# Optimization experiments

Measured on AMD Instinct MI355X. Metric: run time of the kernel, lower is better.

## Reference

```python
import jax, jax.numpy as jnp
import numpy as np

N_NODES = 10000
N_EDGES = 320000
IN_DIM = 256
OUT_DIM = 256
LN_EPS = 1e-5


def setup_inputs() -> dict:
    key = jax.random.key(0)
    ks = jax.random.split(key, 4)
    x = jax.random.normal(ks[0], (N_NODES, IN_DIM), dtype=jnp.float32)
    edge_index = jax.random.randint(ks[1], (2, N_EDGES), 0, N_NODES, dtype=jnp.int64)
    # Linear weights stored input-major so y = x @ W + b
    W_msg = jax.random.normal(ks[2], (2 * IN_DIM, OUT_DIM), dtype=jnp.float32) / np.sqrt(2 * IN_DIM)
    b_msg = jnp.zeros((OUT_DIM,), dtype=jnp.float32)
    W_upd = jax.random.normal(ks[3], (IN_DIM + OUT_DIM, OUT_DIM), dtype=jnp.float32) / np.sqrt(IN_DIM + OUT_DIM)
    b_upd = jnp.zeros((OUT_DIM,), dtype=jnp.float32)
    gamma = jnp.ones((OUT_DIM,), dtype=jnp.float32)
    beta = jnp.zeros((OUT_DIM,), dtype=jnp.float32)
    return {"x": x, "edge_index": edge_index, "W_msg": W_msg, "b_msg": b_msg,
            "W_upd": W_upd, "b_upd": b_upd, "gamma": gamma, "beta": beta}


def reference(x, edge_index, W_msg, b_msg, W_upd, b_upd, gamma, beta):
    row, col = edge_index[0], edge_index[1]
    # gather -> concat -> linear -> relu   [E, out_dim]
    msg_in = jnp.concatenate([x[row], x[col]], axis=-1)
    messages = jax.nn.relu(msg_in @ W_msg + b_msg)
    # scatter-add aggregate over destination nodes  [N, out_dim]
    aggregated = jax.ops.segment_sum(messages, col, num_segments=x.shape[0])
    # update: concat -> linear -> relu -> layernorm
    h = jax.nn.relu(jnp.concatenate([x, aggregated], axis=-1) @ W_upd + b_upd)
    mu = jnp.mean(h, axis=-1, keepdims=True)
    var = jnp.mean(jnp.square(h - mu), axis=-1, keepdims=True)
    return (h - mu) * jax.lax.rsqrt(var + LN_EPS) * gamma + beta
```

## Files before the change

kernel.cpp:

```cpp
#include <hip/hip_runtime.h>
#include <hip/hip_bf16.h>
#include <stdint.h>

#define NNODES 10000
#define NEDGES 320000
#define DIM    256
#define KTOT   512
#define LN_EPS 1e-5f
#define BCAP   96

typedef __attribute__((ext_vector_type(4))) float f32x4;
typedef __attribute__((ext_vector_type(8))) short bf16x8;

__device__ __forceinline__ ushort f2bf(float f) {
    union { float f; uint32_t u; } v; v.f = f;
    uint32_t r = v.u + 0x7fffu + ((v.u >> 16) & 1u);
    return (ushort)(r >> 16);
}
__device__ __forceinline__ float bf2f(ushort u) {
    union { float f; uint32_t u; } v; v.u = ((uint32_t)u) << 16;
    return v.f;
}

__global__ __launch_bounds__(256)
void prep_all(const float* __restrict__ x, const float* __restrict__ Wm,
              const float* __restrict__ Wu, ushort* __restrict__ xb,
              ushort* __restrict__ Wcat, ushort* __restrict__ Wua,
              int4* __restrict__ cntz) {
    int tid = blockIdx.x * 256 + threadIdx.x;
    if (tid < 2560) cntz[tid] = (int4){0, 0, 0, 0};
    if (tid < 640000) {
        float4 v = reinterpret_cast<const float4*>(x)[tid];
        ushort4 o;
        o.x = f2bf(v.x); o.y = f2bf(v.y); o.z = f2bf(v.z); o.w = f2bf(v.w);
        reinterpret_cast<ushort4*>(xb)[tid] = o;
    } else {
        int t = tid - 640000;
        if (t < 131072) {
            int kk  = t >> 14;
            int rem = t & 16383;
            int g   = rem >> 9;
            int kg  = (rem >> 7) & 3;
            int ml  = (rem >> 3) & 15;
            int j   = rem & 7;
            int k = kk * 32 + kg * 8 + j;
            int n = g * 16 + ml;
            float v = (n < 256) ? Wm[k * DIM + n] : Wm[(k + 256) * DIM + (n - 256)];
            Wcat[t] = f2bf(v);
        } else {
            int rem = t - 131072;
            int kk  = rem >> 13;
            int nt  = (rem >> 9) & 15;
            int kg  = (rem >> 7) & 3;
            int ml  = (rem >> 3) & 15;
            int j   = rem & 7;
            int k = kk * 32 + kg * 8 + j;
            int n = nt * 16 + ml;
            Wua[rem] = f2bf(Wu[k * DIM + n]);
        }
    }
}

__global__ __launch_bounds__(256)
void scatter_uv(const int* __restrict__ eidx, int* __restrict__ cnt,
                int* __restrict__ srow, const ushort* __restrict__ xb,
                const ushort* __restrict__ Wcat, const float* __restrict__ bmsg,
                ushort* __restrict__ Ub, float* __restrict__ Vf) {
    if (blockIdx.x < 1250) {
        int e = blockIdx.x * 256 + threadIdx.x;
        int d = eidx[NEDGES + e];
        int p = atomicAdd(&cnt[d], 1);
        if (p < BCAP) srow[d * BCAP + p] = eidx[e];
        return;
    }
    const int wq   = threadIdx.x >> 6;
    const int lane = threadIdx.x & 63;
    const int ml = lane & 15, kg = lane >> 4;
    const int nb = (blockIdx.x - 1250) * 16;
    const uint arow = (uint)(nb + ml) * DIM;

    f32x4 acc[8];
#pragma unroll
    for (int nt = 0; nt < 8; ++nt) acc[nt] = (f32x4){0.f, 0.f, 0.f, 0.f};

#pragma unroll
    for (int kk = 0; kk < 8; ++kk) {
        bf16x8 a = *reinterpret_cast<const bf16x8*>(xb + arow + kk * 32 + kg * 8);
#pragma unroll
        for (int nt = 0; nt < 8; ++nt) {
            bf16x8 b = *reinterpret_cast<const bf16x8*>(Wcat + kk * 16384 + (wq * 8 + nt) * 512 + lane * 8);
            acc[nt] = __builtin_amdgcn_mfma_f32_16x16x32_bf16(a, b, acc[nt], 0, 0, 0);
        }
    }

    if (wq < 2) {
#pragma unroll
        for (int nt = 0; nt < 8; ++nt) {
            const int col = wq * 128 + nt * 16 + ml;
#pragma unroll
            for (int i = 0; i < 4; ++i)
                Ub[(size_t)(nb + kg * 4 + i) * 256 + col] = f2bf(acc[nt][i]);
        }
    } else {
#pragma unroll
        for (int nt = 0; nt < 8; ++nt) {
            const int col = (wq - 2) * 128 + nt * 16 + ml;
            const float bb = bmsg[col];
#pragma unroll
            for (int i = 0; i < 4; ++i)
                Vf[(size_t)(nb + kg * 4 + i) * 256 + col] = acc[nt][i] + bb;
        }
    }
}

__global__ __launch_bounds__(256)
void edge_node(const ushort* __restrict__ Ub, const float* __restrict__ Vf,
               const int* __restrict__ srow, const int* __restrict__ cnt,
               const ushort* __restrict__ xb, const ushort* __restrict__ Wua,
               const float* __restrict__ bupd, const float* __restrict__ gamma,
               const float* __restrict__ beta, float* __restrict__ out) {
    __shared__ float aggS[8][260];
    __shared__ float pS[16][4][2];

    const int tid  = threadIdx.x;
    const int wave = tid >> 6, lane = tid & 63;
    const int nb = blockIdx.x * 8;
    const int el = lane >> 5;
    const int cl = lane & 31;
    const int c0 = cl * 8;

#pragma unroll
    for (int nn = 0; nn < 2; ++nn) {
        const int d = nb + wave * 2 + nn;
        int deg = cnt[d]; deg = deg < BCAP ? deg : BCAP;
        const int beg = d * BCAP;
        const float4 va = *reinterpret_cast<const float4*>(&Vf[(size_t)d * 256 + c0]);
        const float4 vb = *reinterpret_cast<const float4*>(&Vf[(size_t)d * 256 + c0 + 4]);
        float s[8];
#pragma unroll
        for (int j = 0; j < 8; ++j) s[j] = 0.f;

#define ACC8(U) do { \
        s[0] += fmaxf(bf2f((ushort)(U)[0]) + va.x, 0.f); \
        s[1] += fmaxf(bf2f((ushort)(U)[1]) + va.y, 0.f); \
        s[2] += fmaxf(bf2f((ushort)(U)[2]) + va.z, 0.f); \
        s[3] += fmaxf(bf2f((ushort)(U)[3]) + va.w, 0.f); \
        s[4] += fmaxf(bf2f((ushort)(U)[4]) + vb.x, 0.f); \
        s[5] += fmaxf(bf2f((ushort)(U)[5]) + vb.y, 0.f); \
        s[6] += fmaxf(bf2f((ushort)(U)[6]) + vb.z, 0.f); \
        s[7] += fmaxf(bf2f((ushort)(U)[7]) + vb.w, 0.f); } while (0)

        int i = el;
        for (; i + 6 < deg; i += 8) {
            int r0 = srow[beg + i],     r1 = srow[beg + i + 2];
            int r2 = srow[beg + i + 4], r3 = srow[beg + i + 6];
            bf16x8 u0 = *reinterpret_cast<const bf16x8*>(&Ub[(size_t)r0 * 256 + c0]);
            bf16x8 u1 = *reinterpret_cast<const bf16x8*>(&Ub[(size_t)r1 * 256 + c0]);
            bf16x8 u2 = *reinterpret_cast<const bf16x8*>(&Ub[(size_t)r2 * 256 + c0]);
            bf16x8 u3 = *reinterpret_cast<const bf16x8*>(&Ub[(size_t)r3 * 256 + c0]);
            ACC8(u0); ACC8(u1); ACC8(u2); ACC8(u3);
        }
        for (; i < deg; i += 2) {
            int r = srow[beg + i];
            bf16x8 u = *reinterpret_cast<const bf16x8*>(&Ub[(size_t)r * 256 + c0]);
            ACC8(u);
        }
#undef ACC8
#pragma unroll
        for (int j = 0; j < 8; ++j) s[j] += __shfl_xor(s[j], 32);
        if (el == 0) {
            *reinterpret_cast<float4*>(&aggS[wave * 2 + nn][c0])     = (float4){s[0], s[1], s[2], s[3]};
            *reinterpret_cast<float4*>(&aggS[wave * 2 + nn][c0 + 4]) = (float4){s[4], s[5], s[6], s[7]};
        }
    }

    const int ml = lane & 15, kg = lane >> 4, wq = wave;
    const uint arow = (uint)(nb + (ml & 7)) * DIM;

    f32x4 acc[4];
#pragma unroll
    for (int nt = 0; nt < 4; ++nt) acc[nt] = (f32x4){0.f, 0.f, 0.f, 0.f};

#pragma unroll
    for (int kk = 0; kk < 8; ++kk) {
        bf16x8 a = *reinterpret_cast<const bf16x8*>(xb + arow + kk * 32 + kg * 8);
#pragma unroll
        for (int nt = 0; nt < 4; ++nt) {
            bf16x8 b = *reinterpret_cast<const bf16x8*>(Wua + kk * 8192 + (wq * 4 + nt) * 512 + lane * 8);
            acc[nt] = __builtin_amdgcn_mfma_f32_16x16x32_bf16(a, b, acc[nt], 0, 0, 0);
        }
    }
    __syncthreads();

#pragma unroll
    for (int kk = 0; kk < 8; ++kk) {
        float4 f0 = *reinterpret_cast<const float4*>(&aggS[ml & 7][kk * 32 + kg * 8]);
        float4 f1 = *reinterpret_cast<const float4*>(&aggS[ml & 7][kk * 32 + kg * 8 + 4]);
        union { bf16x8 v; __hip_bfloat162 h2[4]; } u;
        u.h2[0] = __float22bfloat162_rn(make_float2(f0.x, f0.y));
        u.h2[1] = __float22bfloat162_rn(make_float2(f0.z, f0.w));
        u.h2[2] = __float22bfloat162_rn(make_float2(f1.x, f1.y));
        u.h2[3] = __float22bfloat162_rn(make_float2(f1.z, f1.w));
#pragma unroll
        for (int nt = 0; nt < 4; ++nt) {
            bf16x8 b = *reinterpret_cast<const bf16x8*>(Wua + 65536 + kk * 8192 + (wq * 4 + nt) * 512 + lane * 8);
            acc[nt] = __builtin_amdgcn_mfma_f32_16x16x32_bf16(u.v, b, acc[nt], 0, 0, 0);
        }
    }

    float sum[4] = {0.f, 0.f, 0.f, 0.f}, ssq[4] = {0.f, 0.f, 0.f, 0.f};
#pragma unroll
    for (int nt = 0; nt < 4; ++nt) {
        const float bb = bupd[(wq * 4 + nt) * 16 + ml];
#pragma unroll
        for (int i = 0; i < 4; ++i) {
            float v = acc[nt][i] + bb;
            v = v > 0.f ? v : 0.f;
            acc[nt][i] = v;
            sum[i] += v;
            ssq[i] += v * v;
        }
    }
#pragma unroll
    for (int m = 1; m < 16; m <<= 1) {
#pragma unroll
        for (int i = 0; i < 4; ++i) {
            sum[i] += __shfl_xor(sum[i], m);
            ssq[i] += __shfl_xor(ssq[i], m);
        }
    }
    if (ml == 0) {
#pragma unroll
        for (int i = 0; i < 4; ++i) {
            pS[kg * 4 + i][wq][0] = sum[i];
            pS[kg * 4 + i][wq][1] = ssq[i];
        }
    }
    __syncthreads();

    float mu[4], rs[4];
#pragma unroll
    for (int i = 0; i < 4; ++i) {
        int r = kg * 4 + i;
        float S = 0.f, Q = 0.f;
#pragma unroll
        for (int w = 0; w < 4; ++w) { S += pS[r][w][0]; Q += pS[r][w][1]; }
        float m = S * (1.f / 256.f);
        float var = Q * (1.f / 256.f) - m * m;
        mu[i] = m;
        rs[i] = rsqrtf(var + LN_EPS);
    }
    if (kg < 2) {
#pragma unroll
        for (int nt = 0; nt < 4; ++nt) {
            const int cc = (wq * 4 + nt) * 16 + ml;
            const float g = gamma[cc], be = beta[cc];
#pragma unroll
            for (int i = 0; i < 4; ++i) {
                const int node = nb + kg * 4 + i;
                out[(size_t)node * DIM + cc] = (acc[nt][i] - mu[i]) * rs[i] * g + be;
            }
        }
    }
}

extern "C" void kernel_launch(void* const* d_in, const int* in_sizes, int n_in,
                              void* d_out, int out_size, void* d_ws, size_t ws_size,
                              hipStream_t stream) {
    const float* x    = (const float*)d_in[0];
    const int*   eidx = (const int*)  d_in[1];
    const float* Wm   = (const float*)d_in[2];
    const float* bm   = (const float*)d_in[3];
    const float* Wu   = (const float*)d_in[4];
    const float* bu   = (const float*)d_in[5];
    const float* gam  = (const float*)d_in[6];
    const float* bet  = (const float*)d_in[7];
    float* out = (float*)d_out;

    char* ws = (char*)d_ws;
    ushort* xb     = (ushort*)(ws);
    ushort* Ub     = (ushort*)(ws +  5120000);
    float*  Vf     = (float*) (ws + 10240000);
    ushort* Wcat   = (ushort*)(ws + 20480000);
    ushort* Wua    = (ushort*)(ws + 20742144);
    int*    cnt    = (int*)   (ws + 21004288);
    int*    srow   = (int*)   (ws + 21045248);

    prep_all<<<3524, 256, 0, stream>>>(x, Wm, Wu, xb, Wcat, Wua, (int4*)cnt);
    scatter_uv<<<1875, 256, 0, stream>>>(eidx, cnt, srow, xb, Wcat, bm, Ub, Vf);
    edge_node<<<NNODES / 8, 256, 0, stream>>>(Ub, Vf, srow, cnt, xb, Wua, bu, gam, bet, out);
}
```

Before: 83.55 us.

## Split edge aggregation from node update GEMM and enlarge GEMM tiles to 64 rows

The fused edge_node kernel becomes two kernels. edge_combine gathers and reduces messages and writes the aggregate to global memory in bf16. node_ln runs the update GEMM plus LayerNorm on 64-node tiles with 512 threads, so each weight fragment is reused across two row tiles. scatter_uv's GEMM part likewise moves to 64-node blocks with 8 waves, and the scatter blocks now leave half their threads idle. The split adds an extra launch and a global round trip for the aggregate, and node_ln runs only 157 blocks, which may underfill the GPU.

```diff
diff --git a/kernel.cpp b/kernel.cpp
--- a/kernel.cpp
+++ b/kernel.cpp
@@ -61,69 +61,84 @@
     }
 }
 
-__global__ __launch_bounds__(256)
+__global__ __launch_bounds__(512)
 void scatter_uv(const int* __restrict__ eidx, int* __restrict__ cnt,
                 int* __restrict__ srow, const ushort* __restrict__ xb,
                 const ushort* __restrict__ Wcat, const float* __restrict__ bmsg,
                 ushort* __restrict__ Ub, float* __restrict__ Vf) {
     if (blockIdx.x < 1250) {
-        int e = blockIdx.x * 256 + threadIdx.x;
-        int d = eidx[NEDGES + e];
-        int p = atomicAdd(&cnt[d], 1);
-        if (p < BCAP) srow[d * BCAP + p] = eidx[e];
+        int e = blockIdx.x * 256 + (threadIdx.x & 255);
+        if (threadIdx.x < 256) {
+            int d = eidx[NEDGES + e];
+            int p = atomicAdd(&cnt[d], 1);
+            if (p < BCAP) srow[d * BCAP + p] = eidx[e];
+        }
         return;
     }
-    const int wq   = threadIdx.x >> 6;
+    const int wave = threadIdx.x >> 6;
     const int lane = threadIdx.x & 63;
     const int ml = lane & 15, kg = lane >> 4;
-    const int nb = (blockIdx.x - 1250) * 16;
-    const uint arow = (uint)(nb + ml) * DIM;
-
-    f32x4 acc[8];
-#pragma unroll
-    for (int nt = 0; nt < 8; ++nt) acc[nt] = (f32x4){0.f, 0.f, 0.f, 0.f};
+    const int wr = wave >> 2, wc = wave & 3;
+    const int nb = (blockIdx.x - 1250) * 64;
+
+    uint arow[2];
+#pragma unroll
+    for (int t = 0; t < 2; ++t) {
+        int n = nb + wr * 32 + t * 16 + ml;
+        arow[t] = (uint)(n < NNODES ? n : NNODES - 1) * DIM;
+    }
+
+    f32x4 acc[2][8];
+#pragma unroll
+    for (int t = 0; t < 2; ++t)
+#pragma unroll
+        for (int nt = 0; nt < 8; ++nt) acc[t][nt] = (f32x4){0.f, 0.f, 0.f, 0.f};
 
 #pragma unroll
     for (int kk = 0; kk < 8; ++kk) {
-        bf16x8 a = *reinterpret_cast<const bf16x8*>(xb + arow + kk * 32 + kg * 8);
+        bf16x8 a0 = *reinterpret_cast<const bf16x8*>(xb + arow[0] + kk * 32 + kg * 8);
+        bf16x8 a1 = *reinterpret_cast<const bf16x8*>(xb + arow[1] + kk * 32 + kg * 8);
 #pragma unroll
         for (int nt = 0; nt < 8; ++nt) {
-            bf16x8 b = *reinterpret_cast<const bf16x8*>(Wcat + kk * 16384 + (wq * 8 + nt) * 512 + lane * 8);
-            acc[nt] = __builtin_amdgcn_mfma_f32_16x16x32_bf16(a, b, acc[nt], 0, 0, 0);
-        }
-    }
-
-    if (wq < 2) {
-#pragma unroll
-        for (int nt = 0; nt < 8; ++nt) {
-            const int col = wq * 128 + nt * 16 + ml;
-#pragma unroll
-            for (int i = 0; i < 4; ++i)
-                Ub[(size_t)(nb + kg * 4 + i) * 256 + col] = f2bf(acc[nt][i]);
-        }
+            bf16x8 b = *reinterpret_cast<const bf16x8*>(Wcat + kk * 16384 + (wc * 8 + nt) * 512 + lane * 8);
+            acc[0][nt] = __builtin_amdgcn_mfma_f32_16x16x32_bf16(a0, b, acc[0][nt], 0, 0, 0);
+            acc[1][nt] = __builtin_amdgcn_mfma_f32_16x16x32_bf16(a1, b, acc[1][nt], 0, 0, 0);
+        }
+    }
+
+    if (wc < 2) {
+#pragma unroll
+        for (int t = 0; t < 2; ++t)
+#pragma unroll
+            for (int nt = 0; nt < 8; ++nt) {
+                const int col = wc * 128 + nt * 16 + ml;
+#pragma unroll
+                for (int i = 0; i < 4; ++i) {
+                    int node = nb + wr * 32 + t * 16 + kg * 4 + i;
+                    if (node < NNODES) Ub[(size_t)node * 256 + col] = f2bf(acc[t][nt][i]);
+                }
+            }
     } else {
 #pragma unroll
-        for (int nt = 0; nt < 8; ++nt) {
-            const int col = (wq - 2) * 128 + nt * 16 + ml;
-            const float bb = bmsg[col];
-#pragma unroll
-            for (int i = 0; i < 4; ++i)
-                Vf[(size_t)(nb + kg * 4 + i) * 256 + col] = acc[nt][i] + bb;
-        }
+        for (int t = 0; t < 2; ++t)
+#pragma unroll
+            for (int nt = 0; nt < 8; ++nt) {
+                const int col = (wc - 2) * 128 + nt * 16 + ml;
+                const float bb = bmsg[col];
+#pragma unroll
+                for (int i = 0; i < 4; ++i) {
+                    int node = nb + wr * 32 + t * 16 + kg * 4 + i;
+                    if (node < NNODES) Vf[(size_t)node * 256 + col] = acc[t][nt][i] + bb;
+                }
+            }
     }
 }
 
 __global__ __launch_bounds__(256)
-void edge_node(const ushort* __restrict__ Ub, const float* __restrict__ Vf,
-               const int* __restrict__ srow, const int* __restrict__ cnt,
-               const ushort* __restrict__ xb, const ushort* __restrict__ Wua,
-               const float* __restrict__ bupd, const float* __restrict__ gamma,
-               const float* __restrict__ beta, float* __restrict__ out) {
-    __shared__ float aggS[8][260];
-    __shared__ float pS[16][4][2];
-
-    const int tid  = threadIdx.x;
-    const int wave = tid >> 6, lane = tid & 63;
+void edge_combine(const ushort* __restrict__ Ub, const float* __restrict__ Vf,
+                  const int* __restrict__ srow, const int* __restrict__ cnt,
+                  ushort* __restrict__ aggb) {
+    const int wave = threadIdx.x >> 6, lane = threadIdx.x & 63;
     const int nb = blockIdx.x * 8;
     const int el = lane >> 5;
     const int cl = lane & 31;
@@ -169,99 +184,130 @@
 #pragma unroll
         for (int j = 0; j < 8; ++j) s[j] += __shfl_xor(s[j], 32);
         if (el == 0) {
-            *reinterpret_cast<float4*>(&aggS[wave * 2 + nn][c0])     = (float4){s[0], s[1], s[2], s[3]};
-            *reinterpret_cast<float4*>(&aggS[wave * 2 + nn][c0 + 4]) = (float4){s[4], s[5], s[6], s[7]};
-        }
-    }
-
-    const int ml = lane & 15, kg = lane >> 4, wq = wave;
-    const uint arow = (uint)(nb + (ml & 7)) * DIM;
-
-    f32x4 acc[4];
-#pragma unroll
-    for (int nt = 0; nt < 4; ++nt) acc[nt] = (f32x4){0.f, 0.f, 0.f, 0.f};
+            union { bf16x8 v; ushort h[8]; } o;
+#pragma unroll
+            for (int j = 0; j < 8; ++j) o.h[j] = f2bf(s[j]);
+            *reinterpret_cast<bf16x8*>(&aggb[(size_t)d * 256 + c0]) = o.v;
+        }
+    }
+}
+
+__global__ __launch_bounds__(512)
+void node_ln(const ushort* __restrict__ xb, const ushort* __restrict__ aggb,
+             const ushort* __restrict__ Wua, const float* __restrict__ bupd,
+             const float* __restrict__ gamma, const float* __restrict__ beta,
+             float* __restrict__ out) {
+    __shared__ float pS[64][4][2];
+
+    const int wave = threadIdx.x >> 6;
+    const int lane = threadIdx.x & 63;
+    const int ml = lane & 15, kg = lane >> 4;
+    const int wr = wave >> 2, wc = wave & 3;
+    const int nb = blockIdx.x * 64;
+
+    uint arow[2];
+#pragma unroll
+    for (int t = 0; t < 2; ++t) {
+        int n = nb + wr * 32 + t * 16 + ml;
+        arow[t] = (uint)(n < NNODES ? n : NNODES - 1) * DIM;
+    }
+
+    f32x4 acc[2][4];
+#pragma unroll
+    for (int t = 0; t < 2; ++t)
+#pragma unroll
+        for (int nt = 0; nt < 4; ++nt) acc[t][nt] = (f32x4){0.f, 0.f, 0.f, 0.f};
 
 #pragma unroll
     for (int kk = 0; kk < 8; ++kk) {
-        bf16x8 a = *reinterpret_cast<const bf16x8*>(xb + arow + kk * 32 + kg * 8);
+        bf16x8 a0 = *reinterpret_cast<const bf16x8*>(xb + arow[0] + kk * 32 + kg * 8);
+        bf16x8 a1 = *reinterpret_cast<const bf16x8*>(xb + arow[1] + kk * 32 + kg * 8);
 #pragma unroll
         for (int nt = 0; nt < 4; ++nt) {
-            bf16x8 b = *reinterpret_cast<const bf16x8*>(Wua + kk * 8192 + (wq * 4 + nt) * 512 + lane * 8);
-            acc[nt] = __builtin_amdgcn_mfma_f32_16x16x32_bf16(a, b, acc[nt], 0, 0, 0);
-        }
+            bf16x8 b = *reinterpret_cast<const bf16x8*>(Wua + kk * 8192 + (wc * 4 + nt) * 512 + lane * 8);
+            acc[0][nt] = __builtin_amdgcn_mfma_f32_16x16x32_bf16(a0, b, acc[0][nt], 0, 0, 0);
+            acc[1][nt] = __builtin_amdgcn_mfma_f32_16x16x32_bf16(a1, b, acc[1][nt], 0, 0, 0);
+        }
+    }
+#pragma unroll
+    for (int kk = 0; kk < 8; ++kk) {
+        bf16x8 a0 = *reinterpret_cast<const bf16x8*>(aggb + arow[0] + kk * 32 + kg * 8);
+        bf16x8 a1 = *reinterpret_cast<const bf16x8*>(aggb + arow[1] + kk * 32 + kg * 8);
+#pragma unroll
+        for (int nt = 0; nt < 4; ++nt) {
+            bf16x8 b = *reinterpret_cast<const bf16x8*>(Wua + 65536 + kk * 8192 + (wc * 4 + nt) * 512 + lane * 8);
+            acc[0][nt] = __builtin_amdgcn_mfma_f32_16x16x32_bf16(a0, b, acc[0][nt], 0, 0, 0);
+            acc[1][nt] = __builtin_amdgcn_mfma_f32_16x16x32_bf16(a1, b, acc[1][nt], 0, 0, 0);
+        }
+    }
+
+    float sum[2][4], ssq[2][4];
+#pragma unroll
+    for (int t = 0; t < 2; ++t)
+#pragma unroll
+        for (int i = 0; i < 4; ++i) { sum[t][i] = 0.f; ssq[t][i] = 0.f; }
+#pragma unroll
+    for (int t = 0; t < 2; ++t)
+#pragma unroll
+        for (int nt = 0; nt < 4; ++nt) {
+            const float bb = bupd[wc * 64 + nt * 16 + ml];
+#pragma unroll
+            for (int i = 0; i < 4; ++i) {
+                float v = acc[t][nt][i] + bb;
+                v = v > 0.f ? v : 0.f;
+                acc[t][nt][i] = v;
+                sum[t][i] += v;
+                ssq[t][i] += v * v;
+            }
+        }
+#pragma unroll
+    for (int m = 1; m < 16; m <<= 1) {
+#pragma unroll
+        for (int t = 0; t < 2; ++t)
+#pragma unroll
+            for (int i = 0; i < 4; ++i) {
+                sum[t][i] += __shfl_xor(sum[t][i], m);
+                ssq[t][i] += __shfl_xor(ssq[t][i], m);
+            }
+    }
+    if (ml == 0) {
+#pragma unroll
+        for (int t = 0; t < 2; ++t)
+#pragma unroll
+            for (int i = 0; i < 4; ++i) {
+                int nl = wr * 32 + t * 16 + kg * 4 + i;
+                pS[nl][wc][0] = sum[t][i];
+                pS[nl][wc][1] = ssq[t][i];
+            }
     }
     __syncthreads();
 
-#pragma unroll
-    for (int kk = 0; kk < 8; ++kk) {
-        float4 f0 = *reinterpret_cast<const float4*>(&aggS[ml & 7][kk * 32 + kg * 8]);
-        float4 f1 = *reinterpret_cast<const float4*>(&aggS[ml & 7][kk * 32 + kg * 8 + 4]);
-        union { bf16x8 v; __hip_bfloat162 h2[4]; } u;
-        u.h2[0] = __float22bfloat162_rn(make_float2(f0.x, f0.y));
-        u.h2[1] = __float22bfloat162_rn(make_float2(f0.z, f0.w));
-        u.h2[2] = __float22bfloat162_rn(make_float2(f1.x, f1.y));
-        u.h2[3] = __float22bfloat162_rn(make_float2(f1.z, f1.w));
+    float mu[2][4], rs[2][4];
+#pragma unroll
+    for (int t = 0; t < 2; ++t)
+#pragma unroll
+        for (int i = 0; i < 4; ++i) {
+            int nl = wr * 32 + t * 16 + kg * 4 + i;
+            float S = pS[nl][0][0] + pS[nl][1][0] + pS[nl][2][0] + pS[nl][3][0];
+            float Q = pS[nl][0][1] + pS[nl][1][1] + pS[nl][2][1] + pS[nl][3][1];
+            float m = S * (1.f / 256.f);
+            float var = Q * (1.f / 256.f) - m * m;
+            mu[t][i] = m;
+            rs[t][i] = rsqrtf(var + LN_EPS);
+        }
+#pragma unroll
+    for (int t = 0; t < 2; ++t)
 #pragma unroll
         for (int nt = 0; nt < 4; ++nt) {
-            bf16x8 b = *reinterpret_cast<const bf16x8*>(Wua + 65536 + kk * 8192 + (wq * 4 + nt) * 512 + lane * 8);
-            acc[nt] = __builtin_amdgcn_mfma_f32_16x16x32_bf16(u.v, b, acc[nt], 0, 0, 0);
-        }
-    }
-
-    float sum[4] = {0.f, 0.f, 0.f, 0.f}, ssq[4] = {0.f, 0.f, 0.f, 0.f};
-#pragma unroll
-    for (int nt = 0; nt < 4; ++nt) {
-        const float bb = bupd[(wq * 4 + nt) * 16 + ml];
-#pragma unroll
-        for (int i = 0; i < 4; ++i) {
-            float v = acc[nt][i] + bb;
-            v = v > 0.f ? v : 0.f;
-            acc[nt][i] = v;
-            sum[i] += v;
-            ssq[i] += v * v;
-        }
-    }
-#pragma unroll
-    for (int m = 1; m < 16; m <<= 1) {
-#pragma unroll
-        for (int i = 0; i < 4; ++i) {
-            sum[i] += __shfl_xor(sum[i], m);
-            ssq[i] += __shfl_xor(ssq[i], m);
-        }
-    }
-    if (ml == 0) {
-#pragma unroll
-        for (int i = 0; i < 4; ++i) {
-            pS[kg * 4 + i][wq][0] = sum[i];
-            pS[kg * 4 + i][wq][1] = ssq[i];
-        }
-    }
-    __syncthreads();
-
-    float mu[4], rs[4];
-#pragma unroll
-    for (int i = 0; i < 4; ++i) {
-        int r = kg * 4 + i;
-        float S = 0.f, Q = 0.f;
-#pragma unroll
-        for (int w = 0; w < 4; ++w) { S += pS[r][w][0]; Q += pS[r][w][1]; }
-        float m = S * (1.f / 256.f);
-        float var = Q * (1.f / 256.f) - m * m;
-        mu[i] = m;
-        rs[i] = rsqrtf(var + LN_EPS);
-    }
-    if (kg < 2) {
-#pragma unroll
-        for (int nt = 0; nt < 4; ++nt) {
-            const int cc = (wq * 4 + nt) * 16 + ml;
+            const int cc = wc * 64 + nt * 16 + ml;
             const float g = gamma[cc], be = beta[cc];
 #pragma unroll
             for (int i = 0; i < 4; ++i) {
-                const int node = nb + kg * 4 + i;
-                out[(size_t)node * DIM + cc] = (acc[nt][i] - mu[i]) * rs[i] * g + be;
-            }
-        }
-    }
+                const int node = nb + wr * 32 + t * 16 + kg * 4 + i;
+                if (node < NNODES)
+                    out[(size_t)node * DIM + cc] = (acc[t][nt][i] - mu[t][i]) * rs[t][i] * g + be;
+            }
+        }
 }
 
 extern "C" void kernel_launch(void* const* d_in, const int* in_sizes, int n_in,
@@ -281,12 +327,14 @@
     ushort* xb     = (ushort*)(ws);
     ushort* Ub     = (ushort*)(ws +  5120000);
     float*  Vf     = (float*) (ws + 10240000);
-    ushort* Wcat   = (ushort*)(ws + 20480000);
-    ushort* Wua    = (ushort*)(ws + 20742144);
-    int*    cnt    = (int*)   (ws + 21004288);
-    int*    srow   = (int*)   (ws + 21045248);
+    ushort* aggb   = (ushort*)(ws + 20480000);
+    ushort* Wcat   = (ushort*)(ws + 25600000);
+    ushort* Wua    = (ushort*)(ws + 25862144);
+    int*    cnt    = (int*)   (ws + 26124288);
+    int*    srow   = (int*)   (ws + 26165248);
 
     prep_all<<<3524, 256, 0, stream>>>(x, Wm, Wu, xb, Wcat, Wua, (int4*)cnt);
-    scatter_uv<<<1875, 256, 0, stream>>>(eidx, cnt, srow, xb, Wcat, bm, Ub, Vf);
-    edge_node<<<NNODES / 8, 256, 0, stream>>>(Ub, Vf, srow, cnt, xb, Wua, bu, gam, bet, out);
-}
+    scatter_uv<<<1407, 512, 0, stream>>>(eidx, cnt, srow, xb, Wcat, bm, Ub, Vf);
+    edge_combine<<<1250, 256, 0, stream>>>(Ub, Vf, srow, cnt, aggb);
+    node_ln<<<157, 512, 0, stream>>>(xb, aggb, Wua, bu, gam, bet, out);
+}
```

Result: slower. 87.41 us (+4.6%).
